# Kernel tuning notes

Hardware: AMD Instinct MI355X
Metric: run time of the kernel (lower is better)

The kernel has to match this reference:

```python
import jax, jax.numpy as jnp
import numpy as np
from jax import lax

B, H, W, C = 8, 64, 64, 256
OUT = 1024          # channels (final conv filters)
KS = 3              # kernel_size
GROUP_DIV = 1
N_GROUPS = C // GROUP_DIV  # 256 -> depthwise-style grouped convs
DN = ('NHWC', 'HWIO', 'NHWC')
EPS = 1e-5


def setup_inputs() -> dict:
    key = jax.random.key(0)
    ks = jax.random.split(key, 6)
    x = jax.random.normal(ks[0], (B, H, W, C), jnp.float32)
    w_spatial = jax.random.normal(ks[1], (B, KS, KS, C // N_GROUPS, C), jnp.float32) * 0.05
    w_pointwise = jax.random.normal(ks[2], (B, 1, 1, C // N_GROUPS, C), jnp.float32) * 0.05
    bias = jax.random.normal(ks[3], (B, C), jnp.float32) * 0.05
    conv_w = jax.random.normal(ks[4], (KS, KS, C, OUT), jnp.float32) * (1.0 / np.sqrt(KS * KS * C))
    conv_b = jnp.zeros((OUT,), jnp.float32)
    return {"x": x, "w_spatial": w_spatial, "w_pointwise": w_pointwise,
            "bias": bias, "conv_w": conv_w, "conv_b": conv_b}


def _instance_norm(x):
    # TF: (x - mean) / (std + eps), population std over H,W per sample/channel
    mean = jnp.mean(x, axis=(1, 2), keepdims=True)
    std = jnp.sqrt(jnp.mean((x - mean) ** 2, axis=(1, 2), keepdims=True))
    return (x - mean) / (std + EPS)


def _per_sample(xi, ws, wp, b):
    # xi: [H,W,C]; ws: [ks,ks,1,C]; wp: [1,1,1,C]; b: [C]
    y = lax.conv_general_dilated(xi[None], ws, (1, 1), 'SAME',
                                 dimension_numbers=DN,
                                 feature_group_count=N_GROUPS)
    y = lax.conv_general_dilated(y, wp, (1, 1), 'VALID',
                                 dimension_numbers=DN,
                                 feature_group_count=N_GROUPS) + b
    return y[0]


def reference(x, w_spatial, w_pointwise, bias, conv_w, conv_b):
    x = _instance_norm(x)
    # batched per-sample dynamic grouped spatial + pointwise conv
    x = jax.vmap(_per_sample)(x, w_spatial, w_pointwise, bias)  # [B,H,W,C]
    # shared 3x3 SAME conv C -> OUT with bias
    y = lax.conv_general_dilated(x, conv_w, (1, 1), 'SAME',
                                 dimension_numbers=DN) + conv_b
    return y
```

## Files before the change

### kernel.cpp

```cpp
#include <hip/hip_runtime.h>
#include <hip/hip_bf16.h>
#include <cstdint>
#include <cstddef>

constexpr int Bn   = 8;
constexpr int Hn   = 64;
constexpr int Wn   = 64;
constexpr int Cn   = 256;
constexpr int OUTC = 1024;
constexpr int HPAD = 66;
constexpr int WPAD = 66;
#define EPS 1e-5f

typedef __attribute__((ext_vector_type(4))) float f32x4;
typedef __bf16 bf16x8 __attribute__((ext_vector_type(8)));

__device__ __forceinline__ void gload_lds16(const void* g, void* l) {
    __builtin_amdgcn_global_load_lds(
        (__attribute__((address_space(1))) void*)g,
        (__attribute__((address_space(3))) void*)l,
        16, 0, 0);
}

__global__ __launch_bounds__(256) void k0_transpose_w(const float* __restrict__ conv_w,
                                                      __hip_bfloat16* __restrict__ wT) {
    __shared__ float tile[64][65];
    const int tap = blockIdx.x;
    const int ct  = blockIdx.y;
    const int ot  = blockIdx.z;
    const int t   = threadIdx.x;
    const int lo  = t & 63;
    const int cq  = t >> 6;

#pragma unroll
    for (int k = 0; k < 16; ++k) {
        int ci = k * 4 + cq;
        tile[lo][ci] = conv_w[((size_t)(tap * Cn + ct * 64 + ci)) * OUTC + ot * 64 + lo];
    }
    __syncthreads();
#pragma unroll
    for (int k = 0; k < 16; ++k) {
        int oo = k * 4 + cq;
        wT[((size_t)(tap * OUTC + ot * 64 + oo)) * Cn + ct * 64 + lo] =
            __float2bfloat16(tile[oo][lo]);
    }
}

__global__ __launch_bounds__(1024) void k1_stats_partial(const float* __restrict__ x,
                                                         float* __restrict__ ps,
                                                         float* __restrict__ pq) {
    __shared__ float sb[2][4][256];
    const int bh = blockIdx.x;
    const int tid = threadIdx.x;
    const int c = tid & 255;
    const int s = tid >> 8;
    const float* row = x + (size_t)bh * Wn * Cn + (size_t)s * 16 * Cn + c;
    float sm = 0.f, q = 0.f;
#pragma unroll
    for (int w = 0; w < 16; ++w) {
        float v = row[(size_t)w * Cn];
        sm += v; q += v * v;
    }
    sb[0][s][c] = sm; sb[1][s][c] = q;
    __syncthreads();
    if (s == 0) {
        float S = 0.f, Q = 0.f;
#pragma unroll
        for (int k = 0; k < 4; ++k) { S += sb[0][k][c]; Q += sb[1][k][c]; }
        ps[bh * Cn + c] = S;
        pq[bh * Cn + c] = Q;
    }
}

__global__ __launch_bounds__(1024) void k2_stats_final(const float* __restrict__ ps,
                                                       const float* __restrict__ pq,
                                                       float* __restrict__ scale,
                                                       float* __restrict__ shift) {
    __shared__ float sb[2][4][256];
    const int b = blockIdx.x;
    const int tid = threadIdx.x;
    const int c = tid & 255;
    const int qd = tid >> 8;
    float S = 0.f, Q = 0.f;
#pragma unroll 4
    for (int i = 0; i < 16; ++i) {
        int h = qd * 16 + i;
        S += ps[(b * Hn + h) * Cn + c];
        Q += pq[(b * Hn + h) * Cn + c];
    }
    sb[0][qd][c] = S; sb[1][qd][c] = Q;
    __syncthreads();
    if (qd == 0) {
        float s2 = 0.f, q2 = 0.f;
#pragma unroll
        for (int k = 0; k < 4; ++k) { s2 += sb[0][k][c]; q2 += sb[1][k][c]; }
        const float inv = 1.f / (float)(Hn * Wn);
        float mean = s2 * inv;
        float var  = fmaxf(q2 * inv - mean * mean, 0.f);
        float sc   = 1.f / (sqrtf(var) + EPS);
        scale[b * Cn + c] = sc;
        shift[b * Cn + c] = -mean * sc;
    }
}

__global__ __launch_bounds__(256) void k3_dwconv(const float* __restrict__ x,
                                                 const float* __restrict__ w_sp,
                                                 const float* __restrict__ w_pw,
                                                 const float* __restrict__ bias,
                                                 const float* __restrict__ scale,
                                                 const float* __restrict__ shift,
                                                 __hip_bfloat16* __restrict__ tpad) {
    const int bq = blockIdx.x;
    const int wq = bq & 3;
    const int bh = bq >> 2;
    const int b  = bh / HPAD;
    const int hp = bh - b * HPAD;
    const int c  = threadIdx.x;
    __hip_bfloat16* orow = tpad + ((size_t)(b * HPAD + hp)) * WPAD * Cn + c;
    const __hip_bfloat16 z = __float2bfloat16(0.f);

    if (hp == 0 || hp == HPAD - 1) {
        int wlo = wq * 17, whi = wlo + 17 < WPAD ? wlo + 17 : WPAD;
        for (int wp = wlo; wp < whi; ++wp) orow[(size_t)wp * Cn] = z;
        return;
    }
    const int h = hp - 1;
    const float sc = scale[b * Cn + c];
    const float sh = shift[b * Cn + c];
    float w9[9];
#pragma unroll
    for (int k = 0; k < 9; ++k) w9[k] = w_sp[(b * 9 + k) * Cn + c];
    const float pw = w_pw[b * Cn + c];
    const float bv = bias[b * Cn + c];
    const float* xb = x + (size_t)b * Hn * Wn * Cn + c;

    bool rv[3];
#pragma unroll
    for (int r = 0; r < 3; ++r) { int rr = h - 1 + r; rv[r] = (rr >= 0 && rr < Hn); }

    if (wq == 0) orow[0] = z;
    if (wq == 3) orow[(size_t)(WPAD - 1) * Cn] = z;

    const int w0 = wq * 16;
    float win[3][3];
#pragma unroll
    for (int r = 0; r < 3; ++r) {
        win[r][0] = (rv[r] && w0 > 0)
                    ? (xb[((size_t)(h - 1 + r) * Wn + (w0 - 1)) * Cn] * sc + sh) : 0.f;
        win[r][1] = rv[r] ? (xb[((size_t)(h - 1 + r) * Wn + w0) * Cn] * sc + sh) : 0.f;
    }
    for (int i = 0; i < 16; ++i) {
        const int w = w0 + i;
#pragma unroll
        for (int r = 0; r < 3; ++r)
            win[r][2] = (rv[r] && (w + 1) < Wn)
                        ? (xb[((size_t)(h - 1 + r) * Wn + (w + 1)) * Cn] * sc + sh) : 0.f;
        float y = 0.f;
#pragma unroll
        for (int r = 0; r < 3; ++r)
#pragma unroll
            for (int qq = 0; qq < 3; ++qq)
                y += win[r][qq] * w9[r * 3 + qq];
        orow[(size_t)(w + 1) * Cn] = __float2bfloat16(y * pw + bv);
#pragma unroll
        for (int r = 0; r < 3; ++r) { win[r][0] = win[r][1]; win[r][1] = win[r][2]; }
    }
}

constexpr int KSTEPS = 72;
constexpr int AREG   = 20480;
constexpr int BUFSZ  = 40960;

__global__ __launch_bounds__(512, 2) void k4_gemm(const __hip_bfloat16* __restrict__ tpad,
                                                  const __hip_bfloat16* __restrict__ wT,
                                                  const float* __restrict__ conv_b,
                                                  float* __restrict__ out) {
    __shared__ __align__(16) char smem[3 * BUFSZ];

    const int tid  = threadIdx.x;
    const int lane = tid & 63;
    const int wv   = tid >> 6;
    const int wm   = wv >> 2;
    const int wn   = wv & 3;
    const int g    = lane >> 4, l15 = lane & 15;

    const int bid = blockIdx.x;
    const int mt  = (bid & 7) * 16 + ((bid >> 3) & 15);
    const int nt  = bid >> 7;
    const int pixbase = mt * 256;
    const int b       = mt >> 4;
    const int hbase   = (mt & 15) * 4;
    const int obase   = nt * 256;

    int off5[5];
#pragma unroll
    for (int j = 0; j < 5; ++j) {
        int u = j * 512 + tid;
        if (u < 1280) {
            int row = u / 5, rs = u - row * 5;
            int ls  = (rs == 4) ? 0 : rs;
            int h   = hbase + (row >> 6);
            int w   = row & 63;
            off5[j] = ((b * HPAD + h) * WPAD + w) * Cn + ls * 8;
        } else {
            int v = u - 1280;
            int row = v / 5, rs = v - row * 5;
            int ls  = (rs == 4) ? 0 : rs;
            off5[j] = (obase + row) * Cn + ls * 8;
        }
    }

    auto stageJ = [&](int s, int j0, int j1) {
        const int tap = s >> 3, ks = s & 7;
        const int kh  = (tap * 11) >> 5;
        const int kw  = tap - kh * 3;
        const __hip_bfloat16* aS = tpad + ((kh * WPAD + kw) * Cn + ks * 32);
        const __hip_bfloat16* bS = wT + (size_t)tap * (OUTC * Cn) + ks * 32;
        char* buf = smem + (s % 3) * BUFSZ;
#pragma unroll
        for (int j = 0; j < 5; ++j) {
            if (j < j0 || j > j1) continue;
            const __hip_bfloat16* src;
            if (j <= 1)      src = aS + off5[j];
            else if (j == 2) src = (tid < 256 ? aS : bS) + off5[j];
            else             src = bS + off5[j];
            gload_lds16(src, buf + (size_t)(j * 512 + wv * 64) * 16);
        }
    };

    f32x4 acc[8][4] = {};

    stageJ(0, 0, 4);
    stageJ(1, 0, 4);
    asm volatile("s_waitcnt vmcnt(5)" ::: "memory");
    __builtin_amdgcn_s_barrier();
    __builtin_amdgcn_sched_barrier(0);

#pragma unroll 1
    for (int t = 0; t < KSTEPS; ++t) {
        char* Ab = smem + (t % 3) * BUFSZ;
        char* Bb = Ab + AREG;
        const bool pf = (t + 2 < KSTEPS);

        bf16x8 bfr[4];
        bf16x8 af[4];

#pragma unroll
        for (int n = 0; n < 4; ++n) {
            int row = wn * 64 + n * 16 + l15;
            bfr[n] = *(const bf16x8*)(Bb + row * 80 + g * 16);
        }
#pragma unroll
        for (int m = 0; m < 4; ++m) {
            int row = wm * 128 + m * 16 + l15;
            af[m] = *(const bf16x8*)(Ab + row * 80 + g * 16);
        }
        if (pf) stageJ(t + 2, 0, 2);
        __builtin_amdgcn_s_barrier();
        __builtin_amdgcn_sched_barrier(0);
        __builtin_amdgcn_s_setprio(1);
#pragma unroll
        for (int m = 0; m < 4; ++m)
#pragma unroll
            for (int n = 0; n < 4; ++n)
                acc[m][n] = __builtin_amdgcn_mfma_f32_16x16x32_bf16(
                    af[m], bfr[n], acc[m][n], 0, 0, 0);
        __builtin_amdgcn_s_setprio(0);
        __builtin_amdgcn_s_barrier();
        __builtin_amdgcn_sched_barrier(0);

#pragma unroll
        for (int m = 0; m < 4; ++m) {
            int row = wm * 128 + (m + 4) * 16 + l15;
            af[m] = *(const bf16x8*)(Ab + row * 80 + g * 16);
        }
        if (pf) stageJ(t + 2, 3, 4);
        __builtin_amdgcn_s_barrier();
        __builtin_amdgcn_sched_barrier(0);
        __builtin_amdgcn_s_setprio(1);
#pragma unroll
        for (int m = 0; m < 4; ++m)
#pragma unroll
            for (int n = 0; n < 4; ++n)
                acc[m + 4][n] = __builtin_amdgcn_mfma_f32_16x16x32_bf16(
                    af[m], bfr[n], acc[m + 4][n], 0, 0, 0);
        __builtin_amdgcn_s_setprio(0);

        if (pf)                      { asm volatile("s_waitcnt vmcnt(5)" ::: "memory"); }
        else if (t + 1 < KSTEPS)     { asm volatile("s_waitcnt vmcnt(0)" ::: "memory"); }
        __builtin_amdgcn_s_barrier();
        __builtin_amdgcn_sched_barrier(0);
    }

    float cb[4];
#pragma unroll
    for (int n = 0; n < 4; ++n) cb[n] = conv_b[obase + wn * 64 + n * 16 + l15];
#pragma unroll
    for (int m = 0; m < 8; ++m) {
#pragma unroll
        for (int j = 0; j < 4; ++j) {
            int r = pixbase + wm * 128 + m * 16 + g * 4 + j;
            float* orow = out + (size_t)r * OUTC + obase + wn * 64 + l15;
#pragma unroll
            for (int n = 0; n < 4; ++n)
                orow[n * 16] = acc[m][n][j] + cb[n];
        }
    }
}

extern "C" void kernel_launch(void* const* d_in, const int* in_sizes, int n_in,
                              void* d_out, int out_size, void* d_ws, size_t ws_size,
                              hipStream_t stream) {
    const float* x      = (const float*)d_in[0];
    const float* w_sp   = (const float*)d_in[1];
    const float* w_pw   = (const float*)d_in[2];
    const float* bias   = (const float*)d_in[3];
    const float* conv_w = (const float*)d_in[4];
    const float* conv_b = (const float*)d_in[5];
    float* out = (float*)d_out;

    char* ws = (char*)d_ws;
    __hip_bfloat16* wT    = (__hip_bfloat16*)(ws);
    float*          ps    = (float*)(ws + 4718592);
    float*          pq    = (float*)(ws + 4718592 + 524288);
    float*          scale = (float*)(ws + 5767168);
    float*          shift = (float*)(ws + 5775360);
    __hip_bfloat16* tpad  = (__hip_bfloat16*)(ws + 5783552);

    k0_transpose_w<<<dim3(9, 4, 16), 256, 0, stream>>>(conv_w, wT);
    k1_stats_partial<<<Bn * Hn, 1024, 0, stream>>>(x, ps, pq);
    k2_stats_final<<<Bn, 1024, 0, stream>>>(ps, pq, scale, shift);
    k3_dwconv<<<Bn * HPAD * 4, 256, 0, stream>>>(x, w_sp, w_pw, bias, scale, shift, tpad);
    k4_gemm<<<512, 512, 0, stream>>>(tpad, wT, conv_b, out);
}
```

Measured before the change: 203.6 us.

## Use XOR-swizzled LDS layout and 4-stage buffer with one barrier per k-step

The implicit-GEMM conv kernel replaces its padded 80-byte-row LDS layout and 3-buffer ring with an unpadded, XOR-swizzled layout, packing two pixels/outputs per 128-byte row, and a 4-buffer ring. Each k-step now waits on vmcnt and then hits a single barrier at the top, instead of three barriers split across two MFMA halves. All 8 A fragments are loaded at once. The aim is to cut barrier stalls and avoid LDS bank conflicts, at the cost of more registers for the A fragments. LDS grows from 120KB to 128KB per block, which could hurt the two-blocks-per-CU occupancy target.

```diff
diff --git a/kernel.cpp b/kernel.cpp
--- a/kernel.cpp
+++ b/kernel.cpp
@@ -168,14 +168,13 @@
 }
 
 constexpr int KSTEPS = 72;
-constexpr int AREG   = 20480;
-constexpr int BUFSZ  = 40960;
+constexpr int BUFSZ  = 32768;
 
 __global__ __launch_bounds__(512, 2) void k4_gemm(const __hip_bfloat16* __restrict__ tpad,
                                                   const __hip_bfloat16* __restrict__ wT,
                                                   const float* __restrict__ conv_b,
                                                   float* __restrict__ out) {
-    __shared__ __align__(16) char smem[3 * BUFSZ];
+    __shared__ __align__(16) char smem[4 * BUFSZ];
 
     const int tid  = threadIdx.x;
     const int lane = tid & 63;
@@ -192,104 +191,73 @@
     const int hbase   = (mt & 15) * 4;
     const int obase   = nt * 256;
 
-    int off5[5];
-#pragma unroll
-    for (int j = 0; j < 5; ++j) {
+    int aoff[2], boff[2];
+#pragma unroll
+    for (int j = 0; j < 2; ++j) {
         int u = j * 512 + tid;
-        if (u < 1280) {
-            int row = u / 5, rs = u - row * 5;
-            int ls  = (rs == 4) ? 0 : rs;
-            int h   = hbase + (row >> 6);
-            int w   = row & 63;
-            off5[j] = ((b * HPAD + h) * WPAD + w) * Cn + ls * 8;
-        } else {
-            int v = u - 1280;
-            int row = v / 5, rs = v - row * 5;
-            int ls  = (rs == 4) ? 0 : rs;
-            off5[j] = (obase + row) * Cn + ls * 8;
-        }
-    }
-
-    auto stageJ = [&](int s, int j0, int j1) {
+        int r = u >> 3, p = u & 7;
+        int l = p ^ (r & 7);
+        int pix = 2 * r + (l >> 2);
+        int hh  = hbase + (pix >> 6);
+        int ww  = pix & 63;
+        aoff[j] = ((b * HPAD + hh) * WPAD + ww) * Cn + (l & 3) * 8;
+        boff[j] = (obase + 2 * r + (l >> 2)) * Cn + (l & 3) * 8;
+    }
+
+    auto stageS = [&](int s) {
         const int tap = s >> 3, ks = s & 7;
-        const int kh  = (tap * 11) >> 5;
-        const int kw  = tap - kh * 3;
+        const int kh  = tap / 3, kw = tap - 3 * kh;
         const __hip_bfloat16* aS = tpad + ((kh * WPAD + kw) * Cn + ks * 32);
         const __hip_bfloat16* bS = wT + (size_t)tap * (OUTC * Cn) + ks * 32;
-        char* buf = smem + (s % 3) * BUFSZ;
-#pragma unroll
-        for (int j = 0; j < 5; ++j) {
-            if (j < j0 || j > j1) continue;
-            const __hip_bfloat16* src;
-            if (j <= 1)      src = aS + off5[j];
-            else if (j == 2) src = (tid < 256 ? aS : bS) + off5[j];
-            else             src = bS + off5[j];
-            gload_lds16(src, buf + (size_t)(j * 512 + wv * 64) * 16);
-        }
+        char* buf = smem + (s & 3) * BUFSZ;
+        gload_lds16(aS + aoff[0], buf + (size_t)(0 * 512 + wv * 64) * 16);
+        gload_lds16(aS + aoff[1], buf + (size_t)(1 * 512 + wv * 64) * 16);
+        gload_lds16(bS + boff[0], buf + 16384 + (size_t)(0 * 512 + wv * 64) * 16);
+        gload_lds16(bS + boff[1], buf + 16384 + (size_t)(1 * 512 + wv * 64) * 16);
     };
 
     f32x4 acc[8][4] = {};
 
-    stageJ(0, 0, 4);
-    stageJ(1, 0, 4);
-    asm volatile("s_waitcnt vmcnt(5)" ::: "memory");
-    __builtin_amdgcn_s_barrier();
-    __builtin_amdgcn_sched_barrier(0);
+    stageS(0);
+    stageS(1);
 
 #pragma unroll 1
     for (int t = 0; t < KSTEPS; ++t) {
-        char* Ab = smem + (t % 3) * BUFSZ;
-        char* Bb = Ab + AREG;
-        const bool pf = (t + 2 < KSTEPS);
-
-        bf16x8 bfr[4];
-        bf16x8 af[4];
-
-#pragma unroll
-        for (int n = 0; n < 4; ++n) {
-            int row = wn * 64 + n * 16 + l15;
-            bfr[n] = *(const bf16x8*)(Bb + row * 80 + g * 16);
-        }
-#pragma unroll
-        for (int m = 0; m < 4; ++m) {
-            int row = wm * 128 + m * 16 + l15;
-            af[m] = *(const bf16x8*)(Ab + row * 80 + g * 16);
-        }
-        if (pf) stageJ(t + 2, 0, 2);
+        if (t < KSTEPS - 1) { asm volatile("s_waitcnt vmcnt(4)" ::: "memory"); }
+        else                { asm volatile("s_waitcnt vmcnt(0)" ::: "memory"); }
+        __builtin_amdgcn_sched_barrier(0);
         __builtin_amdgcn_s_barrier();
         __builtin_amdgcn_sched_barrier(0);
+
+        char* Ab = smem + (t & 3) * BUFSZ;
+        char* Bb = Ab + 16384;
+
+        bf16x8 bfr[4], af[8];
+#pragma unroll
+        for (int n = 0; n < 4; ++n) {
+            int o = wn * 64 + n * 16 + l15;
+            int r = o >> 1;
+            bfr[n] = *(const bf16x8*)(Bb + r * 128 +
+                         ((((o & 1) << 2) | g) ^ (r & 7)) * 16);
+        }
+#pragma unroll
+        for (int m = 0; m < 8; ++m) {
+            int pix = wm * 128 + m * 16 + l15;
+            int r = pix >> 1;
+            af[m] = *(const bf16x8*)(Ab + r * 128 +
+                         ((((pix & 1) << 2) | g) ^ (r & 7)) * 16);
+        }
+
+        if (t + 2 < KSTEPS) stageS(t + 2);
+
         __builtin_amdgcn_s_setprio(1);
 #pragma unroll
-        for (int m = 0; m < 4; ++m)
+        for (int m = 0; m < 8; ++m)
 #pragma unroll
             for (int n = 0; n < 4; ++n)
                 acc[m][n] = __builtin_amdgcn_mfma_f32_16x16x32_bf16(
                     af[m], bfr[n], acc[m][n], 0, 0, 0);
         __builtin_amdgcn_s_setprio(0);
-        __builtin_amdgcn_s_barrier();
-        __builtin_amdgcn_sched_barrier(0);
-
-#pragma unroll
-        for (int m = 0; m < 4; ++m) {
-            int row = wm * 128 + (m + 4) * 16 + l15;
-            af[m] = *(const bf16x8*)(Ab + row * 80 + g * 16);
-        }
-        if (pf) stageJ(t + 2, 3, 4);
-        __builtin_amdgcn_s_barrier();
-        __builtin_amdgcn_sched_barrier(0);
-        __builtin_amdgcn_s_setprio(1);
-#pragma unroll
-        for (int m = 0; m < 4; ++m)
-#pragma unroll
-            for (int n = 0; n < 4; ++n)
-                acc[m + 4][n] = __builtin_amdgcn_mfma_f32_16x16x32_bf16(
-                    af[m], bfr[n], acc[m + 4][n], 0, 0, 0);
-        __builtin_amdgcn_s_setprio(0);
-
-        if (pf)                      { asm volatile("s_waitcnt vmcnt(5)" ::: "memory"); }
-        else if (t + 1 < KSTEPS)     { asm volatile("s_waitcnt vmcnt(0)" ::: "memory"); }
-        __builtin_amdgcn_s_barrier();
-        __builtin_amdgcn_sched_barrier(0);
     }
 
     float cb[4];
```

Result: faster. 176.5 us (-13.3%).
